# Performance work log

Hardware: AMD Instinct MI355X
Metric: run time of the kernel (lower is better)

## Reference

```python
import jax, jax.numpy as jnp
import numpy as np

B, S, D, H, DFF = 2, 4096, 512, 8, 2048
DK = D // H
EPS = 1e-6


def layer_norm(x, alpha, bias):
    # torch: (x - mean) / (std + eps), std unbiased (ddof=1), eps added to std
    mean = jnp.mean(x, axis=-1, keepdims=True)
    std = jnp.std(x, axis=-1, keepdims=True, ddof=1)
    return alpha * (x - mean) / (std + EPS) + bias


def setup_inputs() -> dict:
    key = jax.random.key(0)
    ks = jax.random.split(key, 10)
    s = 0.02
    return {
        "x": jax.random.normal(ks[0], (B, S, D), jnp.float32),
        "mask": jax.random.randint(ks[1], (S, S), 0, 2, jnp.int32),
        "w_q": jax.random.normal(ks[2], (D, D), jnp.float32) * s,
        "w_k": jax.random.normal(ks[3], (D, D), jnp.float32) * s,
        "w_v": jax.random.normal(ks[4], (D, D), jnp.float32) * s,
        "w_o": jax.random.normal(ks[5], (D, D), jnp.float32) * s,
        "w1": jax.random.normal(ks[6], (D, DFF), jnp.float32) * s,
        "b1": jnp.zeros((DFF,), jnp.float32),
        "w2": jax.random.normal(ks[7], (DFF, D), jnp.float32) * s,
        "b2": jnp.zeros((D,), jnp.float32),
        "ln1_a": jnp.ones((D,), jnp.float32),
        "ln1_b": jnp.zeros((D,), jnp.float32),
        "ln2_a": jnp.ones((D,), jnp.float32),
        "ln2_b": jnp.zeros((D,), jnp.float32),
    }


def reference(x, mask, w_q, w_k, w_v, w_o, w1, b1, w2, b2, ln1_a, ln1_b, ln2_a, ln2_b):
    # --- sublayer 0: pre-norm self-attention with residual (dropout=0/eval) ---
    h = layer_norm(x, ln1_a, ln1_b)                       # [B,S,D]
    q = (h @ w_q).reshape(B, S, H, DK)
    k = (h @ w_k).reshape(B, S, H, DK)
    v = (h @ w_v).reshape(B, S, H, DK)
    scores = jnp.einsum("bqhd,bkhd->bhqk", q, k) / jnp.sqrt(jnp.float32(DK))
    scores = jnp.where(mask[None, None, :, :] == 0, jnp.float32(-1e9), scores)
    attn = jax.nn.softmax(scores, axis=-1)                # [B,H,S,S]
    ctx = jnp.einsum("bhqk,bkhd->bqhd", attn, v).reshape(B, S, D)
    x = x + ctx @ w_o
    # --- sublayer 1: pre-norm FFN with residual ---
    h2 = layer_norm(x, ln2_a, ln2_b)
    ff = jax.nn.relu(h2 @ w1 + b1) @ w2 + b2
    return x + ff
```

## Files before the change

kernel.cpp:

```cpp
#include <hip/hip_runtime.h>
#include <hip/hip_bf16.h>
#include <stdint.h>

#define S_LEN 4096
#define DMODEL 512
#define NHEAD 8
#define DHEAD 64
#define NTOK 8192

typedef unsigned short ushort_t;
typedef __attribute__((ext_vector_type(8))) short short8;
typedef __attribute__((ext_vector_type(4))) float f32x4;
typedef unsigned long long u64;
typedef __attribute__((ext_vector_type(2))) unsigned uint2v;

__device__ __forceinline__ float bf2f(ushort_t h) {
    union { unsigned u; float f; } c; c.u = ((unsigned)h) << 16; return c.f;
}
__device__ __forceinline__ ushort_t f2bf(float f) {
    union { float f; unsigned u; } c; c.f = f;
    unsigned u = c.u + 0x7fffu + ((c.u >> 16) & 1u);
    return (ushort_t)(u >> 16);
}
__device__ __forceinline__ void glds16(const ushort_t* g, ushort_t* l) {
    __builtin_amdgcn_global_load_lds(
        (const __attribute__((address_space(1))) unsigned int*)g,
        (__attribute__((address_space(3))) unsigned int*)l, 16, 0, 0);
}

__global__ __launch_bounds__(256) void maskbits_kernel(const int* __restrict__ mask,
        u64* __restrict__ mb) {
    size_t id = (size_t)blockIdx.x * 256 + threadIdx.x;
    int v = mask[id];
    u64 bits = __ballot(v != 0);
    if ((threadIdx.x & 63) == 0) mb[id >> 6] = bits;
}

__global__ __launch_bounds__(256) void wtrans_all(const float* __restrict__ wq,
        const float* __restrict__ wk, const float* __restrict__ wv,
        const float* __restrict__ wo, const float* __restrict__ w1,
        const float* __restrict__ w2,
        ushort_t* wqT, ushort_t* wkT, ushort_t* wvT, ushort_t* woT,
        ushort_t* w1T, ushort_t* w2T) {
    __shared__ __attribute__((aligned(16))) ushort_t t[64][72];
    int z = blockIdx.z;
    const float* src; ushort_t* dst; int R, C;
    switch (z) {
        case 0: src = wq; dst = wqT; R = 512;  C = 512;  break;
        case 1: src = wk; dst = wkT; R = 512;  C = 512;  break;
        case 2: src = wv; dst = wvT; R = 512;  C = 512;  break;
        case 3: src = wo; dst = woT; R = 512;  C = 512;  break;
        case 4: src = w1; dst = w1T; R = 512;  C = 2048; break;
        default: src = w2; dst = w2T; R = 2048; C = 512; break;
    }
    int r0 = blockIdx.x * 64, c0 = blockIdx.y * 64;
    if (r0 >= R || c0 >= C) return;
    int tid = threadIdx.x;
    for (int i = tid; i < 4096; i += 256) {
        int r = i >> 6, c = i & 63;
        t[r][c] = f2bf(src[(size_t)(r0 + r) * C + c0 + c]);
    }
    __syncthreads();
    for (int i = tid; i < 512; i += 256) {
        int c = i >> 3, rb = i & 7;
        short8 vv;
#pragma unroll
        for (int j = 0; j < 8; j++) ((ushort_t*)&vv)[j] = t[rb * 8 + j][c];
        *(short8*)(dst + (size_t)(c0 + c) * R + r0 + rb * 8) = vv;
    }
}

__global__ __launch_bounds__(256) void ln_f32(const float* __restrict__ x,
        const float* __restrict__ ga, const float* __restrict__ be,
        ushort_t* __restrict__ out) {
    int tok = blockIdx.x * 4 + (threadIdx.x >> 6);
    int lane = threadIdx.x & 63;
    const float* xr = x + (size_t)tok * DMODEL + lane * 8;
    f32x4 v0 = *(const f32x4*)xr;
    f32x4 v1 = *(const f32x4*)(xr + 4);
    float f[8];
    float s = 0.f, s2 = 0.f;
#pragma unroll
    for (int i = 0; i < 8; i++) {
        f[i] = (i < 4) ? v0[i] : v1[i - 4];
        s += f[i]; s2 += f[i] * f[i];
    }
#pragma unroll
    for (int off = 1; off < 64; off <<= 1) {
        s += __shfl_xor(s, off);
        s2 += __shfl_xor(s2, off);
    }
    float mean = s * (1.f / DMODEL);
    float var = (s2 - (float)DMODEL * mean * mean) * (1.f / (DMODEL - 1));
    var = fmaxf(var, 0.f);
    float inv = 1.f / (sqrtf(var) + 1e-6f);
    short8 o;
#pragma unroll
    for (int i = 0; i < 8; i++) {
        float val = ga[lane * 8 + i] * (f[i] - mean) * inv + be[lane * 8 + i];
        ((ushort_t*)&o)[i] = f2bf(val);
    }
    *(short8*)(out + (size_t)tok * DMODEL + lane * 8) = o;
}

__global__ __launch_bounds__(256) void vtrans(const ushort_t* __restrict__ V,
        ushort_t* __restrict__ VT) {
    __shared__ __attribute__((aligned(16))) ushort_t t[64][72];
    int s0 = blockIdx.x * 64;
    int bh = blockIdx.y;
    int b = bh >> 3, h = bh & 7;
    int tid = threadIdx.x;
    const ushort_t* src = V + ((size_t)b * S_LEN + s0) * DMODEL + h * DHEAD;
    for (int i = tid; i < 512; i += 256) {
        int r = i >> 3, cb = i & 7;
        *(short8*)&t[r][cb * 8] = *(const short8*)(src + (size_t)r * DMODEL + cb * 8);
    }
    __syncthreads();
    ushort_t* dst = VT + (size_t)bh * DHEAD * S_LEN;
    for (int i = tid; i < 512; i += 256) {
        int d = i >> 3, rb = i & 7;
        short8 vv;
#pragma unroll
        for (int j = 0; j < 8; j++) ((ushort_t*)&vv)[j] = t[rb * 8 + j][d];
        *(short8*)(dst + (size_t)d * S_LEN + s0 + rb * 8) = vv;
    }
}

template <int MW, int NW>
__device__ __forceinline__ void gemm_body(const ushort_t* __restrict__ A,
        const ushort_t* __restrict__ BT, void* __restrict__ C,
        int N, int K, float scale, const float* __restrict__ bias,
        const float* __restrict__ res, int relu, int cf32,
        ushort_t* As, ushort_t* Bs, int m0, int n0, int aoff, int coff) {
    int tid = threadIdx.x;
    int wave = tid >> 6, lane = tid & 63;
    int wm = wave >> 1, wn = wave & 1;
    int lr = lane & 15, lg = lane >> 4;
    int srow = lane >> 2, spos = lane & 3;
    int swz = (spos ^ ((srow >> 1) & 3)) * 8;
    int rdw = (lr >> 1) & 3;
    f32x4 acc[MW][NW];
#pragma unroll
    for (int i = 0; i < MW; i++)
#pragma unroll
        for (int j = 0; j < NW; j++) acc[i][j] = (f32x4){0.f, 0.f, 0.f, 0.f};

    const ushort_t* Ag = A + (size_t)(m0 - aoff) * K;
    const ushort_t* Bg = BT + (size_t)n0 * K;

    for (int k0 = 0; k0 < K; k0 += 32) {
        __syncthreads();
        for (int ia = wave; ia < 2 * MW; ia += 4)
            glds16(Ag + (size_t)(ia * 16 + srow) * K + k0 + swz, As + ia * 16 * 32);
        for (int ib = wave; ib < 2 * NW; ib += 4)
            glds16(Bg + (size_t)(ib * 16 + srow) * K + k0 + swz, Bs + ib * 16 * 32);
        __syncthreads();
        short8 af[MW], bfv[NW];
#pragma unroll
        for (int t = 0; t < MW; t++)
            af[t] = *(const short8*)(As + (wm * 16 * MW + t * 16 + lr) * 32 + (lg ^ rdw) * 8);
#pragma unroll
        for (int t = 0; t < NW; t++)
            bfv[t] = *(const short8*)(Bs + (wn * 16 * NW + t * 16 + lr) * 32 + (lg ^ rdw) * 8);
#pragma unroll
        for (int i = 0; i < MW; i++)
#pragma unroll
            for (int j = 0; j < NW; j++)
                acc[i][j] = __builtin_amdgcn_mfma_f32_16x16x32_bf16(af[i], bfv[j], acc[i][j], 0, 0, 0);
    }
#pragma unroll
    for (int i = 0; i < MW; i++) {
        int row = m0 + wm * 16 * MW + i * 16 + lg * 4;
#pragma unroll
        for (int j = 0; j < NW; j++) {
            int col = n0 + wn * 16 * NW + j * 16 + lr;
            float bb = bias ? bias[col] : 0.f;
#pragma unroll
            for (int r = 0; r < 4; r++) {
                float v = acc[i][j][r] * scale + bb;
                if (relu) v = fmaxf(v, 0.f);
                if (res) v += res[(size_t)(row + r) * N + col];
                size_t cidx = (size_t)(row + r - coff) * N + col;
                if (cf32) ((float*)C)[cidx] = v;
                else      ((ushort_t*)C)[cidx] = f2bf(v);
            }
        }
    }
}

__global__ __launch_bounds__(256) void gemm_bt64(const ushort_t* __restrict__ A,
        const ushort_t* __restrict__ BT, void* __restrict__ C,
        int N, int K, float scale, const float* bias, const float* res, int relu,
        int cf32, int m_base, int aoff, int coff) {
    __shared__ __attribute__((aligned(16))) ushort_t As[64 * 32];
    __shared__ __attribute__((aligned(16))) ushort_t Bs[64 * 32];
    gemm_body<2, 2>(A, BT, C, N, K, scale, bias, res, relu, cf32, As, Bs,
                    m_base + blockIdx.x * 64, blockIdx.y * 64, aoff, coff);
}

__global__ __launch_bounds__(256) void gemm_qkv(const ushort_t* __restrict__ A,
        const ushort_t* __restrict__ wqT, const ushort_t* __restrict__ wkT,
        const ushort_t* __restrict__ wvT,
        ushort_t* __restrict__ Q, ushort_t* __restrict__ Kb, ushort_t* __restrict__ V) {
    __shared__ __attribute__((aligned(16))) ushort_t As[128 * 32];
    __shared__ __attribute__((aligned(16))) ushort_t Bs[128 * 32];
    int z = blockIdx.z;
    const ushort_t* W = (z == 0) ? wqT : ((z == 1) ? wkT : wvT);
    ushort_t* O = (z == 0) ? Q : ((z == 1) ? Kb : V);
    float sc = (z == 0) ? 0.18033688011112042f : 1.f;
    gemm_body<4, 4>(A, W, O, DMODEL, DMODEL, sc, nullptr, nullptr, 0, 0, As, Bs,
                    blockIdx.x * 128, blockIdx.y * 128, 0, 0);
}

__global__ __launch_bounds__(128, 4) void attn_kernel(const ushort_t* __restrict__ Q,
        const ushort_t* __restrict__ K, const ushort_t* __restrict__ VT,
        const unsigned* __restrict__ mb32, ushort_t* __restrict__ Opart,
        float* __restrict__ lpart) {
    __shared__ __attribute__((aligned(16))) ushort_t Ks[2][32 * 64];
    __shared__ __attribute__((aligned(16))) ushort_t Vs[2][64 * 32];
    __shared__ __attribute__((aligned(16))) ushort_t Pw[2][32 * 40];
    int qt = blockIdx.x, h = blockIdx.y, zz = blockIdx.z;
    int b = zz >> 1, half = zz & 1;
    int tid = threadIdx.x;
    int wv = __builtin_amdgcn_readfirstlane(tid >> 6);
    int lane = tid & 63;
    int lr = lane & 15, lg = lane >> 4;
    size_t tokbase = (size_t)b * S_LEN;
    int q0 = qt * 64 + wv * 32;
    int k0 = half * (S_LEN / 2);

    const ushort_t* Qp = Q + (tokbase + q0) * DMODEL + h * DHEAD;
    short8 qf[2][2];
#pragma unroll
    for (int u = 0; u < 2; u++) {
        qf[u][0] = *(const short8*)(Qp + (size_t)(u * 16 + lr) * DMODEL + lg * 8);
        qf[u][1] = *(const short8*)(Qp + (size_t)(u * 16 + lr) * DMODEL + 32 + lg * 8);
    }
    f32x4 o[2][4];
#pragma unroll
    for (int u = 0; u < 2; u++)
#pragma unroll
        for (int td = 0; td < 4; td++) o[u][td] = (f32x4){0.f, 0.f, 0.f, 0.f};
    float lsl[2] = {0.f, 0.f};

    int srow = lane >> 3, spos = lane & 7;
    int srow2 = lane >> 2, spos2 = lane & 3;
    int kst = (spos ^ srow) * 8;
    int vst = (spos2 ^ ((srow2 >> 1) & 3)) * 8;
    int rdk = lr & 7;
    int rdv = (lr >> 1) & 3;

    const ushort_t* kgl = K + (tokbase + k0) * DMODEL + h * DHEAD
                          + (size_t)srow * DMODEL + kst;
    const ushort_t* vgl = VT + (size_t)(b * NHEAD + h) * DHEAD * S_LEN
                          + (size_t)srow2 * S_LEN + k0 + vst;
    const unsigned* mr0 = mb32 + (size_t)(q0 + lr) * 128 + half * 64;
    const unsigned* mr1 = mb32 + (size_t)(q0 + 16 + lr) * 128 + half * 64;

    unsigned w0 = mr0[0], w1 = mr1[0];
    if (wv == 0) {
        glds16(kgl + (size_t)0 * DMODEL, &Ks[0][0 * 64]);
        glds16(kgl + (size_t)8 * DMODEL, &Ks[0][8 * 64]);
        glds16(vgl + (size_t)0 * S_LEN, &Vs[0][0 * 32]);
        glds16(vgl + (size_t)16 * S_LEN, &Vs[0][16 * 32]);
    } else {
        glds16(kgl + (size_t)16 * DMODEL, &Ks[0][16 * 64]);
        glds16(kgl + (size_t)24 * DMODEL, &Ks[0][24 * 64]);
        glds16(vgl + (size_t)32 * S_LEN, &Vs[0][32 * 32]);
        glds16(vgl + (size_t)48 * S_LEN, &Vs[0][48 * 32]);
    }

    const int NIT = (S_LEN / 2) / 32;
#pragma unroll 1
    for (int kt = 0; kt < NIT; kt++) {
        int cur = kt & 1;
        __builtin_amdgcn_s_barrier();
        unsigned nw0 = 0, nw1 = 0;
        if (kt + 1 < NIT) {
            nw0 = mr0[kt + 1];
            nw1 = mr1[kt + 1];
            const ushort_t* kgn = kgl + (size_t)(kt + 1) * 32 * DMODEL;
            const ushort_t* vgn = vgl + (kt + 1) * 32;
            if (wv == 0) {
                glds16(kgn + (size_t)0 * DMODEL, &Ks[cur ^ 1][0 * 64]);
                glds16(kgn + (size_t)8 * DMODEL, &Ks[cur ^ 1][8 * 64]);
                glds16(vgn + (size_t)0 * S_LEN, &Vs[cur ^ 1][0 * 32]);
                glds16(vgn + (size_t)16 * S_LEN, &Vs[cur ^ 1][16 * 32]);
            } else {
                glds16(kgn + (size_t)16 * DMODEL, &Ks[cur ^ 1][16 * 64]);
                glds16(kgn + (size_t)24 * DMODEL, &Ks[cur ^ 1][24 * 64]);
                glds16(vgn + (size_t)32 * S_LEN, &Vs[cur ^ 1][32 * 32]);
                glds16(vgn + (size_t)48 * S_LEN, &Vs[cur ^ 1][48 * 32]);
            }
            __builtin_amdgcn_s_waitcnt(3958);
        } else {
            __builtin_amdgcn_s_waitcnt(3952);
        }
        __builtin_amdgcn_s_barrier();
        const ushort_t* Kb_ = Ks[cur];
        const ushort_t* Vb_ = Vs[cur];
        f32x4 s[2][2];
#pragma unroll
        for (int t = 0; t < 2; t++) {
            const ushort_t* kr = Kb_ + (t * 16 + lr) * 64;
            short8 kf0 = *(const short8*)(kr + ((lg ^ rdk) * 8));
            short8 kf1 = *(const short8*)(kr + (((lg + 4) ^ rdk) * 8));
#pragma unroll
            for (int u = 0; u < 2; u++) {
                f32x4 z = (f32x4){0.f, 0.f, 0.f, 0.f};
                z = __builtin_amdgcn_mfma_f32_16x16x32_bf16(kf0, qf[u][0], z, 0, 0, 0);
                z = __builtin_amdgcn_mfma_f32_16x16x32_bf16(kf1, qf[u][1], z, 0, 0, 0);
                s[t][u] = z;
            }
        }
#pragma unroll
        for (int u = 0; u < 2; u++) {
            unsigned wq = (u ? w1 : w0) >> (lg * 4);
#pragma unroll
            for (int r = 0; r < 4; r++) {
                float p0, p1;
                asm("v_exp_f32 %0, %1\n\ts_nop 0" : "=v"(p0) : "v"(s[0][u][r]));
                asm("v_exp_f32 %0, %1\n\ts_nop 0" : "=v"(p1) : "v"(s[1][u][r]));
                p0 = ((wq >> r) & 1u) ? p0 : 0.f;
                p1 = ((wq >> (16 + r)) & 1u) ? p1 : 0.f;
                s[0][u][r] = p0; s[1][u][r] = p1;
                lsl[u] += p0 + p1;
            }
        }
        ushort_t* Pb = Pw[wv];
#pragma unroll
        for (int u = 0; u < 2; u++)
#pragma unroll
            for (int t = 0; t < 2; t++) {
                uint2v pk;
                asm("v_cvt_pk_bf16_f32 %0, %1, %2" : "=v"(pk.x) : "v"(s[t][u][0]), "v"(s[t][u][1]));
                asm("v_cvt_pk_bf16_f32 %0, %1, %2" : "=v"(pk.y) : "v"(s[t][u][2]), "v"(s[t][u][3]));
                *(uint2v*)(Pb + (u * 16 + lr) * 40 + t * 16 + lg * 4) = pk;
            }
        short8 vf[4];
#pragma unroll
        for (int td = 0; td < 4; td++)
            vf[td] = *(const short8*)(Vb_ + (td * 16 + lr) * 32 + ((lg ^ rdv) * 8));
#pragma unroll
        for (int u = 0; u < 2; u++) {
            short8 pf = *(const short8*)(Pb + (u * 16 + lr) * 40 + lg * 8);
#pragma unroll
            for (int td = 0; td < 4; td++)
                o[u][td] = __builtin_amdgcn_mfma_f32_16x16x32_bf16(pf, vf[td], o[u][td], 0, 0, 0);
        }
        w0 = nw0; w1 = nw1;
    }
#pragma unroll
    for (int u = 0; u < 2; u++) {
        lsl[u] += __shfl_xor(lsl[u], 16);
        lsl[u] += __shfl_xor(lsl[u], 32);
    }
    float* lp = lpart + (size_t)half * (NHEAD * 2 * S_LEN)
                + (size_t)(b * NHEAD + h) * S_LEN + q0;
    if (lane < 16) {
        lp[lane] = lsl[0];
        lp[16 + lane] = lsl[1];
    }
    ushort_t* Op = Opart + (size_t)half * NTOK * DMODEL;
#pragma unroll
    for (int u = 0; u < 2; u++) {
        size_t rowb = (tokbase + q0 + u * 16 + lg * 4) * DMODEL + h * DHEAD;
#pragma unroll
        for (int td = 0; td < 4; td++) {
            int cc = td * 16 + lr;
            Op[rowb + 0 * DMODEL + cc] = f2bf(o[u][td][0]);
            Op[rowb + 1 * DMODEL + cc] = f2bf(o[u][td][1]);
            Op[rowb + 2 * DMODEL + cc] = f2bf(o[u][td][2]);
            Op[rowb + 3 * DMODEL + cc] = f2bf(o[u][td][3]);
        }
    }
}

__global__ __launch_bounds__(256) void attn_combine(const ushort_t* __restrict__ Oa,
        const ushort_t* __restrict__ Ob, const float* __restrict__ la,
        const float* __restrict__ lb, ushort_t* __restrict__ ctx) {
    size_t idx = ((size_t)blockIdx.x * 256 + threadIdx.x) * 8;
    size_t tok = idx >> 9;
    int col = (int)(idx & 511);
    int h = col >> 6;
    int b = (int)(tok >> 12);
    int q = (int)(tok & 4095);
    size_t li = (size_t)(b * NHEAD + h) * S_LEN + q;
    float inv = 1.f / (la[li] + lb[li]);
    short8 va = *(const short8*)(Oa + idx);
    short8 vb = *(const short8*)(Ob + idx);
    short8 oo;
#pragma unroll
    for (int j = 0; j < 8; j++)
        ((ushort_t*)&oo)[j] = f2bf((bf2f(((const ushort_t*)&va)[j])
                                  + bf2f(((const ushort_t*)&vb)[j])) * inv);
    *(short8*)(ctx + idx) = oo;
}

extern "C" void kernel_launch(void* const* d_in, const int* in_sizes, int n_in,
                              void* d_out, int out_size, void* d_ws, size_t ws_size,
                              hipStream_t stream) {
    (void)in_sizes; (void)n_in; (void)out_size; (void)ws_size;
    const float* x    = (const float*)d_in[0];
    const int*   mask = (const int*)d_in[1];
    const float* w_q  = (const float*)d_in[2];
    const float* w_k  = (const float*)d_in[3];
    const float* w_v  = (const float*)d_in[4];
    const float* w_o  = (const float*)d_in[5];
    const float* w1   = (const float*)d_in[6];
    const float* b1   = (const float*)d_in[7];
    const float* w2   = (const float*)d_in[8];
    const float* b2   = (const float*)d_in[9];
    const float* l1a  = (const float*)d_in[10];
    const float* l1b  = (const float*)d_in[11];
    const float* l2a  = (const float*)d_in[12];
    const float* l2b  = (const float*)d_in[13];

    char* ws = (char*)d_ws;
    const size_t MB = 1024 * 1024;
    const size_t KB = 1024;
    ushort_t* w1T  = (ushort_t*)(ws + 0);
    ushort_t* w2T  = (ushort_t*)(ws + 2 * MB);
    ushort_t* wqT  = (ushort_t*)(ws + 4 * MB);
    ushort_t* wkT  = (ushort_t*)(ws + 4 * MB + 512 * KB);
    ushort_t* wvT  = (ushort_t*)(ws + 5 * MB);
    ushort_t* woT  = (ushort_t*)(ws + 5 * MB + 512 * KB);
    ushort_t* ff1  = (ushort_t*)(ws + 6 * MB);
    ushort_t* h    = (ushort_t*)(ws + 22 * MB);
    ushort_t* VTb  = h;
    ushort_t* h2   = h;
    ushort_t* Qb   = (ushort_t*)(ws + 30 * MB);
    float*    x2f  = (float*)(ws + 30 * MB);
    ushort_t* Kb   = (ushort_t*)(ws + 38 * MB);
    ushort_t* Vb   = (ushort_t*)(ws + 46 * MB);
    ushort_t* ctx  = Vb;
    ushort_t* Opart = ff1;
    float*    lpart = (float*)wqT;
    u64*      mb   = (u64*)d_out;
    float*    out  = (float*)d_out;

    dim3 blk(256);
    maskbits_kernel<<<dim3(65536), blk, 0, stream>>>(mask, mb);
    wtrans_all<<<dim3(32, 32, 6), blk, 0, stream>>>(w_q, w_k, w_v, w_o, w1, w2,
            wqT, wkT, wvT, woT, w1T, w2T);
    ln_f32<<<dim3(NTOK / 4), blk, 0, stream>>>(x, l1a, l1b, h);
    gemm_qkv<<<dim3(64, 4, 3), blk, 0, stream>>>(h, wqT, wkT, wvT, Qb, Kb, Vb);
    vtrans<<<dim3(64, 16), blk, 0, stream>>>(Vb, VTb);
    attn_kernel<<<dim3(64, 8, 4), dim3(128), 0, stream>>>(Qb, Kb, VTb,
            (const unsigned*)mb, Opart, lpart);
    attn_combine<<<dim3(2048), blk, 0, stream>>>(Opart,
            Opart + (size_t)NTOK * DMODEL, lpart, lpart + NHEAD * 2 * S_LEN, ctx);
    gemm_bt64<<<dim3(128, 8), blk, 0, stream>>>(ctx, woT, x2f, 512, 512, 1.f,
            nullptr, x, 0, 1, 0, 0, 0);
    ln_f32<<<dim3(NTOK / 4), blk, 0, stream>>>(x2f, l2a, l2b, h2);
    gemm_bt64<<<dim3(64, 32), blk, 0, stream>>>(h2, w1T, ff1, 2048, 512, 1.f,
            b1, nullptr, 1, 0, 0, 0, 0);
    gemm_bt64<<<dim3(64, 8), blk, 0, stream>>>(ff1, w2T, out, 512, 2048, 1.f,
            b2, x2f, 0, 1, 0, 0, 0);
    gemm_bt64<<<dim3(64, 32), blk, 0, stream>>>(h2, w1T, ff1, 2048, 512, 1.f,
            b1, nullptr, 1, 0, 4096, 0, 4096);
    gemm_bt64<<<dim3(64, 8), blk, 0, stream>>>(ff1, w2T, out, 512, 2048, 1.f,
            b2, x2f, 0, 1, 4096, 4096, 0);
}
```

Baseline: 453.9 us.

## Use larger GEMM tiles and keep attention P in registers via permlane swaps

```diff
diff --git a/kernel.cpp b/kernel.cpp
--- a/kernel.cpp
+++ b/kernel.cpp
@@ -188,14 +188,24 @@
     }
 }
 
-__global__ __launch_bounds__(256) void gemm_bt64(const ushort_t* __restrict__ A,
+__global__ __launch_bounds__(256) void gemm_bt128(const ushort_t* __restrict__ A,
         const ushort_t* __restrict__ BT, void* __restrict__ C,
         int N, int K, float scale, const float* bias, const float* res, int relu,
         int cf32, int m_base, int aoff, int coff) {
-    __shared__ __attribute__((aligned(16))) ushort_t As[64 * 32];
+    __shared__ __attribute__((aligned(16))) ushort_t As[128 * 32];
+    __shared__ __attribute__((aligned(16))) ushort_t Bs[128 * 32];
+    gemm_body<4, 4>(A, BT, C, N, K, scale, bias, res, relu, cf32, As, Bs,
+                    m_base + blockIdx.x * 128, blockIdx.y * 128, aoff, coff);
+}
+
+__global__ __launch_bounds__(256) void gemm_bt128x64(const ushort_t* __restrict__ A,
+        const ushort_t* __restrict__ BT, void* __restrict__ C,
+        int N, int K, float scale, const float* bias, const float* res, int relu,
+        int cf32, int m_base, int aoff, int coff) {
+    __shared__ __attribute__((aligned(16))) ushort_t As[128 * 32];
     __shared__ __attribute__((aligned(16))) ushort_t Bs[64 * 32];
-    gemm_body<2, 2>(A, BT, C, N, K, scale, bias, res, relu, cf32, As, Bs,
-                    m_base + blockIdx.x * 64, blockIdx.y * 64, aoff, coff);
+    gemm_body<4, 2>(A, BT, C, N, K, scale, bias, res, relu, cf32, As, Bs,
+                    m_base + blockIdx.x * 128, blockIdx.y * 64, aoff, coff);
 }
 
 __global__ __launch_bounds__(256) void gemm_qkv(const ushort_t* __restrict__ A,
@@ -218,7 +228,6 @@
         float* __restrict__ lpart) {
     __shared__ __attribute__((aligned(16))) ushort_t Ks[2][32 * 64];
     __shared__ __attribute__((aligned(16))) ushort_t Vs[2][64 * 32];
-    __shared__ __attribute__((aligned(16))) ushort_t Pw[2][32 * 40];
     int qt = blockIdx.x, h = blockIdx.y, zz = blockIdx.z;
     int b = zz >> 1, half = zz & 1;
     int tid = threadIdx.x;
@@ -241,7 +250,10 @@
     for (int u = 0; u < 2; u++)
 #pragma unroll
         for (int td = 0; td < 4; td++) o[u][td] = (f32x4){0.f, 0.f, 0.f, 0.f};
-    float lsl[2] = {0.f, 0.f};
+    f32x4 den[2] = {(f32x4){0.f, 0.f, 0.f, 0.f}, (f32x4){0.f, 0.f, 0.f, 0.f}};
+    short8 ones8;
+#pragma unroll
+    for (int j = 0; j < 8; j++) ((ushort_t*)&ones8)[j] = 0x3F80;
 
     int srow = lane >> 3, spos = lane & 7;
     int srow2 = lane >> 2, spos2 = lane & 3;
@@ -324,42 +336,41 @@
                 p0 = ((wq >> r) & 1u) ? p0 : 0.f;
                 p1 = ((wq >> (16 + r)) & 1u) ? p1 : 0.f;
                 s[0][u][r] = p0; s[1][u][r] = p1;
-                lsl[u] += p0 + p1;
             }
         }
-        ushort_t* Pb = Pw[wv];
-#pragma unroll
-        for (int u = 0; u < 2; u++)
-#pragma unroll
-            for (int t = 0; t < 2; t++) {
-                uint2v pk;
-                asm("v_cvt_pk_bf16_f32 %0, %1, %2" : "=v"(pk.x) : "v"(s[t][u][0]), "v"(s[t][u][1]));
-                asm("v_cvt_pk_bf16_f32 %0, %1, %2" : "=v"(pk.y) : "v"(s[t][u][2]), "v"(s[t][u][3]));
-                *(uint2v*)(Pb + (u * 16 + lr) * 40 + t * 16 + lg * 4) = pk;
-            }
         short8 vf[4];
 #pragma unroll
         for (int td = 0; td < 4; td++)
             vf[td] = *(const short8*)(Vb_ + (td * 16 + lr) * 32 + ((lg ^ rdv) * 8));
 #pragma unroll
         for (int u = 0; u < 2; u++) {
-            short8 pf = *(const short8*)(Pb + (u * 16 + lr) * 40 + lg * 8);
+            unsigned c00, c01, c10, c11;
+            asm("v_cvt_pk_bf16_f32 %0, %1, %2" : "=v"(c00) : "v"(s[0][u][0]), "v"(s[0][u][1]));
+            asm("v_cvt_pk_bf16_f32 %0, %1, %2" : "=v"(c01) : "v"(s[0][u][2]), "v"(s[0][u][3]));
+            asm("v_cvt_pk_bf16_f32 %0, %1, %2" : "=v"(c10) : "v"(s[1][u][0]), "v"(s[1][u][1]));
+            asm("v_cvt_pk_bf16_f32 %0, %1, %2" : "=v"(c11) : "v"(s[1][u][2]), "v"(s[1][u][3]));
+            auto r0 = __builtin_amdgcn_permlane32_swap(c00, c10, false, false);
+            auto r1 = __builtin_amdgcn_permlane32_swap(c01, c11, false, false);
+            auto p0 = __builtin_amdgcn_permlane16_swap(r0[0], r0[1], false, false);
+            auto p1 = __builtin_amdgcn_permlane16_swap(r1[0], r1[1], false, false);
+            union { unsigned u32[4]; short8 s8; } pk;
+            pk.u32[0] = p0[0]; pk.u32[1] = p1[0]; pk.u32[2] = p0[1]; pk.u32[3] = p1[1];
+            short8 pf = pk.s8;
 #pragma unroll
             for (int td = 0; td < 4; td++)
                 o[u][td] = __builtin_amdgcn_mfma_f32_16x16x32_bf16(pf, vf[td], o[u][td], 0, 0, 0);
+            den[u] = __builtin_amdgcn_mfma_f32_16x16x32_bf16(pf, ones8, den[u], 0, 0, 0);
         }
         w0 = nw0; w1 = nw1;
-    }
-#pragma unroll
-    for (int u = 0; u < 2; u++) {
-        lsl[u] += __shfl_xor(lsl[u], 16);
-        lsl[u] += __shfl_xor(lsl[u], 32);
     }
     float* lp = lpart + (size_t)half * (NHEAD * 2 * S_LEN)
                 + (size_t)(b * NHEAD + h) * S_LEN + q0;
-    if (lane < 16) {
-        lp[lane] = lsl[0];
-        lp[16 + lane] = lsl[1];
+    if (lr == 0) {
+#pragma unroll
+        for (int u = 0; u < 2; u++)
+#pragma unroll
+            for (int r = 0; r < 4; r++)
+                lp[u * 16 + lg * 4 + r] = den[u][r];
     }
     ushort_t* Op = Opart + (size_t)half * NTOK * DMODEL;
 #pragma unroll
@@ -450,15 +461,15 @@
             (const unsigned*)mb, Opart, lpart);
     attn_combine<<<dim3(2048), blk, 0, stream>>>(Opart,
             Opart + (size_t)NTOK * DMODEL, lpart, lpart + NHEAD * 2 * S_LEN, ctx);
-    gemm_bt64<<<dim3(128, 8), blk, 0, stream>>>(ctx, woT, x2f, 512, 512, 1.f,
+    gemm_bt128<<<dim3(64, 4), blk, 0, stream>>>(ctx, woT, x2f, 512, 512, 1.f,
             nullptr, x, 0, 1, 0, 0, 0);
     ln_f32<<<dim3(NTOK / 4), blk, 0, stream>>>(x2f, l2a, l2b, h2);
-    gemm_bt64<<<dim3(64, 32), blk, 0, stream>>>(h2, w1T, ff1, 2048, 512, 1.f,
+    gemm_bt128<<<dim3(32, 16), blk, 0, stream>>>(h2, w1T, ff1, 2048, 512, 1.f,
             b1, nullptr, 1, 0, 0, 0, 0);
-    gemm_bt64<<<dim3(64, 8), blk, 0, stream>>>(ff1, w2T, out, 512, 2048, 1.f,
+    gemm_bt128x64<<<dim3(32, 8), blk, 0, stream>>>(ff1, w2T, out, 512, 2048, 1.f,
             b2, x2f, 0, 1, 0, 0, 0);
-    gemm_bt64<<<dim3(64, 32), blk, 0, stream>>>(h2, w1T, ff1, 2048, 512, 1.f,
+    gemm_bt128<<<dim3(32, 16), blk, 0, stream>>>(h2, w1T, ff1, 2048, 512, 1.f,
             b1, nullptr, 1, 0, 4096, 0, 4096);
-    gemm_bt64<<<dim3(64, 8), blk, 0, stream>>>(ff1, w2T, out, 512, 2048, 1.f,
+    gemm_bt128x64<<<dim3(32, 8), blk, 0, stream>>>(ff1, w2T, out, 512, 2048, 1.f,
             b2, x2f, 0, 1, 4096, 4096, 0);
 }
```

New measurement: 464.8 us. 1.02x slower.
